# Kernel tuning notes

Hardware: AMD Instinct MI355X
Metric: run time of the kernel (lower is better)

Reference implementation:

```python
import jax, jax.numpy as jnp
import numpy as np

N = 100000   # nodes
E = 1600000  # edges
DIN = 128
HID = 128
D2 = 64      # hard-coded last-conv width in the module
OUT = 1000


def setup_inputs() -> dict:
    key = jax.random.key(0)
    ks = jax.random.split(key, 8)
    x = jax.random.normal(ks[0], (N, DIN), dtype=jnp.float32)
    edge_index = jax.random.randint(ks[1], (2, E), 0, N, dtype=jnp.int64)
    W1 = jax.random.normal(ks[2], (DIN, HID), dtype=jnp.float32) * 0.05
    b1 = jnp.zeros((HID,), dtype=jnp.float32)
    W2 = jax.random.normal(ks[3], (HID, D2), dtype=jnp.float32) * 0.05
    b2 = jnp.zeros((D2,), dtype=jnp.float32)
    Wfc = jax.random.normal(ks[4], (D2, OUT), dtype=jnp.float32) * 0.05
    bfc = jnp.zeros((OUT,), dtype=jnp.float32)
    return {"x": x, "W1": W1, "b1": b1, "W2": W2, "b2": b2,
            "Wfc": Wfc, "bfc": bfc, "edge_index": edge_index}


def _gcn_conv(x, W, b, src, dst):
    # PyG GCNConv: h = X W; add self-loops; symmetric norm D^-1/2 (A+I) D^-1/2; + bias
    h = x @ W                                   # [N, F]
    ones = jnp.ones(src.shape[0], dtype=h.dtype)
    deg = jax.ops.segment_sum(ones, dst, num_segments=N) + 1.0  # +1 for self-loop
    dinv = jax.lax.rsqrt(deg)                   # [N]
    norm = dinv[src] * dinv[dst]                # [E]
    agg = jax.ops.segment_sum(h[src] * norm[:, None], dst, num_segments=N)
    agg = agg + h * (dinv * dinv)[:, None]      # self-loop contribution
    return agg + b


def reference(x, W1, b1, W2, b2, Wfc, bfc, edge_index):
    src, dst = edge_index[0], edge_index[1]
    h = jax.nn.relu(_gcn_conv(x, W1, b1, src, dst))
    # dropout is identity in eval mode (training=False)
    h = jax.nn.relu(_gcn_conv(h, W2, b2, src, dst))
    return h @ Wfc + bfc
```

## Files before the change

### kernel.cpp

```cpp
#include <hip/hip_runtime.h>
#include <hip/hip_bf16.h>
#include <cstddef>

typedef __attribute__((ext_vector_type(8))) short bf16x8;
typedef __attribute__((ext_vector_type(4))) float f32x4;

__device__ __forceinline__ unsigned short f2bf(float f) {
    __hip_bfloat16 h = __float2bfloat16(f);
    return __builtin_bit_cast(unsigned short, h);
}
__device__ __forceinline__ float bf2f(unsigned short u) {
    return __bfloat162float(__builtin_bit_cast(__hip_bfloat16, u));
}
__device__ __forceinline__ float bflo(unsigned u) {
    return __builtin_bit_cast(float, u << 16);
}
__device__ __forceinline__ float bfhi(unsigned u) {
    return __builtin_bit_cast(float, u & 0xffff0000u);
}


__global__ void k_zero_i(int* __restrict__ p, int total) {
    int i = blockIdx.x * blockDim.x + threadIdx.x;
    int stride = gridDim.x * blockDim.x;
    for (; i < total; i += stride) p[i] = 0;
}


__global__ void k_deg_i(const int* __restrict__ dst, int* __restrict__ deg, int E) {
    int e = blockIdx.x * blockDim.x + threadIdx.x;
    if (e < E) atomicAdd(&deg[dst[e]], 1);
}

__global__ void k_dinv(const int* __restrict__ deg, float* __restrict__ dinv, int N) {
    int i = blockIdx.x * blockDim.x + threadIdx.x;
    if (i < N) dinv[i] = rsqrtf((float)deg[i] + 1.0f);
}


#define SCAN_B 1024

__global__ void k_scan1(const int* __restrict__ in, int* __restrict__ out,
                        int* __restrict__ sums, int n) {
    __shared__ int tmp[SCAN_B];
    int tid = threadIdx.x;
    int gid = blockIdx.x * SCAN_B + tid;
    int v = (gid < n) ? in[gid] : 0;
    tmp[tid] = v;
    __syncthreads();
    for (int off = 1; off < SCAN_B; off <<= 1) {
        int t = (tid >= off) ? tmp[tid - off] : 0;
        __syncthreads();
        tmp[tid] += t;
        __syncthreads();
    }
    if (gid < n) out[gid] = tmp[tid] - v;
    if (tid == SCAN_B - 1) sums[blockIdx.x] = tmp[tid];
}

__global__ void k_scan2(int* __restrict__ sums, int nb) {
    __shared__ int tmp[128];
    int tid = threadIdx.x;
    int v = (tid < nb) ? sums[tid] : 0;
    tmp[tid] = v;
    __syncthreads();
    for (int off = 1; off < 128; off <<= 1) {
        int t = (tid >= off) ? tmp[tid - off] : 0;
        __syncthreads();
        tmp[tid] += t;
        __syncthreads();
    }
    if (tid < nb) sums[tid] = tmp[tid] - v;
}

__global__ void k_scan3(int* __restrict__ out, int* __restrict__ cursor,
                        const int* __restrict__ sums, int n) {
    int gid = blockIdx.x * SCAN_B + threadIdx.x;
    if (gid < n) {
        int v = out[gid] + sums[blockIdx.x];
        out[gid] = v;
        cursor[gid] = v;
    }
}


__global__ void k_fill(const int* __restrict__ src, const int* __restrict__ dst,
                       int* __restrict__ cursor, int* __restrict__ csr_src, int E) {
    int e = blockIdx.x * blockDim.x + threadIdx.x;
    if (e < E) {
        int pos = atomicAdd(&cursor[dst[e]], 1);
        csr_src[pos] = src[e];
    }
}


__global__ void k_conv_w_bf(const float* __restrict__ W, unsigned short* __restrict__ Bh,
                            int K, int N)
{
    int n = blockIdx.x;
    int k = threadIdx.x;
    Bh[(size_t)n * K + k] = f2bf(W[(size_t)k * N + n]);
}

__global__ void k_conv_w(const float* __restrict__ W, unsigned short* __restrict__ Bh,
                         unsigned short* __restrict__ Bl, int K, int N)
{
    int n = blockIdx.x;
    int k = threadIdx.x;
    float v = W[(size_t)k * N + n];
    unsigned short hi = f2bf(v);
    unsigned short lo = f2bf(v - bf2f(hi));
    Bh[(size_t)n * K + k] = hi;
    Bl[(size_t)n * K + k] = lo;
}


__device__ __forceinline__ void unpack_fma(float* a, float w, uint4 v) {
    a[0] = fmaf(w, bflo(v.x), a[0]);
    a[1] = fmaf(w, bfhi(v.x), a[1]);
    a[2] = fmaf(w, bflo(v.y), a[2]);
    a[3] = fmaf(w, bfhi(v.y), a[3]);
    a[4] = fmaf(w, bflo(v.z), a[4]);
    a[5] = fmaf(w, bfhi(v.z), a[5]);
    a[6] = fmaf(w, bflo(v.w), a[6]);
    a[7] = fmaf(w, bfhi(v.w), a[7]);
}

__launch_bounds__(256)
__global__ void k_gather128(const unsigned short* __restrict__ hbf,
                            const int* __restrict__ csr_src, const int* __restrict__ off,
                            const float* __restrict__ dinv, const float* __restrict__ bias,
                            unsigned short* __restrict__ obf, int N, int E)
{
    int node = blockIdx.x * 4 + (threadIdx.x >> 6);
    int lane = threadIdx.x & 63;
    if (node >= N) return;
    float dn = dinv[node];
    int beg = off[node];
    int end = (node + 1 < N) ? off[node + 1] : E;

    const int grp = lane >> 4;
    const int sub = lane & 15;

    float a[8] = {0.f, 0.f, 0.f, 0.f, 0.f, 0.f, 0.f, 0.f};
    int i = beg + grp;
    for (; i + 4 < end; i += 8) {
        int s0 = csr_src[i];
        int s1 = csr_src[i + 4];
        float w0 = dinv[s0] * dn;
        float w1 = dinv[s1] * dn;
        uint4 v0 = *(const uint4*)(hbf + (size_t)s0 * 128 + sub * 8);
        uint4 v1 = *(const uint4*)(hbf + (size_t)s1 * 128 + sub * 8);
        unpack_fma(a, w0, v0);
        unpack_fma(a, w1, v1);
    }
    if (i < end) {
        int s = csr_src[i];
        float w = dinv[s] * dn;
        uint4 v = *(const uint4*)(hbf + (size_t)s * 128 + sub * 8);
        unpack_fma(a, w, v);
    }

#pragma unroll
    for (int k = 0; k < 8; ++k) {
        a[k] += __shfl_xor(a[k], 16);
        a[k] += __shfl_xor(a[k], 32);
    }

    if (grp == 0) {
        uint4 sv = *(const uint4*)(hbf + (size_t)node * 128 + sub * 8);
        float s[8] = {bflo(sv.x), bfhi(sv.x), bflo(sv.y), bfhi(sv.y),
                      bflo(sv.z), bfhi(sv.z), bflo(sv.w), bfhi(sv.w)};
        float4 b0 = *(const float4*)(bias + sub * 8);
        float4 b1 = *(const float4*)(bias + sub * 8 + 4);
        float bv[8] = {b0.x, b0.y, b0.z, b0.w, b1.x, b1.y, b1.z, b1.w};
        float w = dn * dn;
        unsigned short o[8];
#pragma unroll
        for (int k = 0; k < 8; ++k)
            o[k] = f2bf(fmaxf(fmaf(s[k], w, a[k]) + bv[k], 0.f));
        uint4 vo;
        vo.x = (unsigned)o[0] | ((unsigned)o[1] << 16);
        vo.y = (unsigned)o[2] | ((unsigned)o[3] << 16);
        vo.z = (unsigned)o[4] | ((unsigned)o[5] << 16);
        vo.w = (unsigned)o[6] | ((unsigned)o[7] << 16);
        *(uint4*)(obf + (size_t)node * 128 + sub * 8) = vo;
    }
}


__launch_bounds__(256)
__global__ void k_gather64(const unsigned short* __restrict__ hbf,
                           const int* __restrict__ csr_src, const int* __restrict__ off,
                           const float* __restrict__ dinv, const float* __restrict__ bias,
                           unsigned short* __restrict__ hhi, unsigned short* __restrict__ hlo,
                           int N, int E)
{
    int node = blockIdx.x * 4 + (threadIdx.x >> 6);
    int lane = threadIdx.x & 63;
    if (node >= N) return;
    float dn = dinv[node];
    int beg = off[node];
    int end = (node + 1 < N) ? off[node + 1] : E;

    const int grp = lane >> 3;
    const int sub = lane & 7;

    float a[8] = {0.f, 0.f, 0.f, 0.f, 0.f, 0.f, 0.f, 0.f};
    int i = beg + grp;
    for (; i + 8 < end; i += 16) {
        int s0 = csr_src[i];
        int s1 = csr_src[i + 8];
        float w0 = dinv[s0] * dn;
        float w1 = dinv[s1] * dn;
        uint4 v0 = *(const uint4*)(hbf + (size_t)s0 * 64 + sub * 8);
        uint4 v1 = *(const uint4*)(hbf + (size_t)s1 * 64 + sub * 8);
        unpack_fma(a, w0, v0);
        unpack_fma(a, w1, v1);
    }
    if (i < end) {
        int s = csr_src[i];
        float w = dinv[s] * dn;
        uint4 v = *(const uint4*)(hbf + (size_t)s * 64 + sub * 8);
        unpack_fma(a, w, v);
    }

#pragma unroll
    for (int k = 0; k < 8; ++k) {
        a[k] += __shfl_xor(a[k], 8);
        a[k] += __shfl_xor(a[k], 16);
        a[k] += __shfl_xor(a[k], 32);
    }

    if (grp == 0) {
        uint4 sv = *(const uint4*)(hbf + (size_t)node * 64 + sub * 8);
        float s[8] = {bflo(sv.x), bfhi(sv.x), bflo(sv.y), bfhi(sv.y),
                      bflo(sv.z), bfhi(sv.z), bflo(sv.w), bfhi(sv.w)};
        float4 b0 = *(const float4*)(bias + sub * 8);
        float4 b1 = *(const float4*)(bias + sub * 8 + 4);
        float bv[8] = {b0.x, b0.y, b0.z, b0.w, b1.x, b1.y, b1.z, b1.w};
        float w = dn * dn;
        unsigned short hi[8], lo[8];
#pragma unroll
        for (int k = 0; k < 8; ++k) {
            float f = fmaxf(fmaf(s[k], w, a[k]) + bv[k], 0.f);
            hi[k] = f2bf(f);
            lo[k] = f2bf(f - bf2f(hi[k]));
        }
        uint4 vh, vl;
        vh.x = (unsigned)hi[0] | ((unsigned)hi[1] << 16);
        vh.y = (unsigned)hi[2] | ((unsigned)hi[3] << 16);
        vh.z = (unsigned)hi[4] | ((unsigned)hi[5] << 16);
        vh.w = (unsigned)hi[6] | ((unsigned)hi[7] << 16);
        vl.x = (unsigned)lo[0] | ((unsigned)lo[1] << 16);
        vl.y = (unsigned)lo[2] | ((unsigned)lo[3] << 16);
        vl.z = (unsigned)lo[4] | ((unsigned)lo[5] << 16);
        vl.w = (unsigned)lo[6] | ((unsigned)lo[7] << 16);
        *(uint4*)(hhi + (size_t)node * 64 + sub * 8) = vh;
        *(uint4*)(hlo + (size_t)node * 64 + sub * 8) = vl;
    }
}


__launch_bounds__(256, 2)
__global__ void gemm_mfma_l1(const float* __restrict__ A,
                             const unsigned short* __restrict__ Bt,
                             unsigned short* __restrict__ Cbf, int M)
{
    __shared__ unsigned short Ah[128 * 64];
    __shared__ unsigned short Bh[128 * 64];

    const int tid = threadIdx.x;
    const int m0 = blockIdx.x * 128;
    const int lane = tid & 63, wave = tid >> 6;
    const int wr = wave >> 1, wc = wave & 1;
    const int lrow = lane & 15, kgrp = lane >> 4;

    f32x4 acc[4][4] = {};

    for (int ph = 0; ph < 2; ++ph) {
        const int k0 = ph * 64;
        __syncthreads();
        {
            const int c4 = tid & 15, r0 = tid >> 4;
#pragma unroll
            for (int p = 0; p < 8; ++p) {
                int row = r0 + p * 16;
                int gr = m0 + row; if (gr >= M) gr = M - 1;
                float4 v = *(const float4*)(A + (size_t)gr * 128 + k0 + c4 * 4);
                ushort4 hv;
                hv.x = f2bf(v.x); hv.y = f2bf(v.y); hv.z = f2bf(v.z); hv.w = f2bf(v.w);
                *(ushort4*)((char*)Ah + row * 128 + ((c4 * 8) ^ ((row & 7) << 4))) = hv;
            }
        }
        {
            const int c = tid & 7, col0 = tid >> 3;
#pragma unroll
            for (int p = 0; p < 4; ++p) {
                int col = col0 + p * 32;
                uint4 v = *(const uint4*)(Bt + (size_t)col * 128 + k0 + c * 8);
                *(uint4*)((char*)Bh + col * 128 + ((c * 16) ^ ((col & 7) << 4))) = v;
            }
        }
        __syncthreads();

#pragma unroll
        for (int ks = 0; ks < 2; ++ks) {
            const int cIdx = kgrp + ks * 4;
            bf16x8 ah[4], bh[4];
#pragma unroll
            for (int i = 0; i < 4; ++i) {
                int row = wr * 64 + i * 16 + lrow;
                ah[i] = *(const bf16x8*)((const char*)Ah + row * 128 + ((cIdx * 16) ^ ((row & 7) << 4)));
            }
#pragma unroll
            for (int j = 0; j < 4; ++j) {
                int col = wc * 64 + j * 16 + lrow;
                bh[j] = *(const bf16x8*)((const char*)Bh + col * 128 + ((cIdx * 16) ^ ((col & 7) << 4)));
            }
#pragma unroll
            for (int i = 0; i < 4; ++i)
#pragma unroll
                for (int j = 0; j < 4; ++j)
                    acc[i][j] = __builtin_amdgcn_mfma_f32_16x16x32_bf16(bh[j], ah[i], acc[i][j], 0, 0, 0);
        }
    }

#pragma unroll
    for (int i = 0; i < 4; ++i) {
        int grow = m0 + wr * 64 + i * 16 + lrow;
        if (grow >= M) continue;
        unsigned short* crow = Cbf + (size_t)grow * 128;
#pragma unroll
        for (int j = 0; j < 4; ++j) {
            int gc = wc * 64 + j * 16 + kgrp * 4;
            ushort4 o;
            o.x = f2bf(acc[i][j][0]);
            o.y = f2bf(acc[i][j][1]);
            o.z = f2bf(acc[i][j][2]);
            o.w = f2bf(acc[i][j][3]);
            *(ushort4*)(crow + gc) = o;
        }
    }
}


__launch_bounds__(256, 3)
__global__ void gemm_mfma_l2(const unsigned short* __restrict__ Abf,
                             const unsigned short* __restrict__ Bt,
                             unsigned short* __restrict__ Cbf, int M)
{
    __shared__ unsigned short Ah[128 * 64];
    __shared__ unsigned short Bh[64 * 64];

    const int tid = threadIdx.x;
    const int m0 = blockIdx.x * 128;
    const int lane = tid & 63, wave = tid >> 6;
    const int wr = wave >> 1, wc = wave & 1;
    const int lrow = lane & 15, kgrp = lane >> 4;

    f32x4 acc[4][2] = {};

    for (int ph = 0; ph < 2; ++ph) {
        const int k0 = ph * 64;
        __syncthreads();
        {
            const int c = tid & 7, r0 = tid >> 3;
#pragma unroll
            for (int p = 0; p < 4; ++p) {
                int row = r0 + p * 32;
                int gr = m0 + row; if (gr >= M) gr = M - 1;
                uint4 v = *(const uint4*)(Abf + (size_t)gr * 128 + k0 + c * 8);
                *(uint4*)((char*)Ah + row * 128 + ((c * 16) ^ ((row & 7) << 4))) = v;
            }
        }
        {
            const int c = tid & 7, col0 = tid >> 3;
#pragma unroll
            for (int p = 0; p < 2; ++p) {
                int col = col0 + p * 32;
                uint4 v = *(const uint4*)(Bt + (size_t)col * 128 + k0 + c * 8);
                *(uint4*)((char*)Bh + col * 128 + ((c * 16) ^ ((col & 7) << 4))) = v;
            }
        }
        __syncthreads();

#pragma unroll
        for (int ks = 0; ks < 2; ++ks) {
            const int cIdx = kgrp + ks * 4;
            bf16x8 ah[4], bh[2];
#pragma unroll
            for (int i = 0; i < 4; ++i) {
                int row = wr * 64 + i * 16 + lrow;
                ah[i] = *(const bf16x8*)((const char*)Ah + row * 128 + ((cIdx * 16) ^ ((row & 7) << 4)));
            }
#pragma unroll
            for (int j = 0; j < 2; ++j) {
                int col = wc * 32 + j * 16 + lrow;
                bh[j] = *(const bf16x8*)((const char*)Bh + col * 128 + ((cIdx * 16) ^ ((col & 7) << 4)));
            }
#pragma unroll
            for (int i = 0; i < 4; ++i)
#pragma unroll
                for (int j = 0; j < 2; ++j)
                    acc[i][j] = __builtin_amdgcn_mfma_f32_16x16x32_bf16(bh[j], ah[i], acc[i][j], 0, 0, 0);
        }
    }

#pragma unroll
    for (int i = 0; i < 4; ++i) {
        int grow = m0 + wr * 64 + i * 16 + lrow;
        if (grow >= M) continue;
        unsigned short* crow = Cbf + (size_t)grow * 64;
#pragma unroll
        for (int j = 0; j < 2; ++j) {
            int gc = wc * 32 + j * 16 + kgrp * 4;
            ushort4 o;
            o.x = f2bf(acc[i][j][0]);
            o.y = f2bf(acc[i][j][1]);
            o.z = f2bf(acc[i][j][2]);
            o.w = f2bf(acc[i][j][3]);
            *(ushort4*)(crow + gc) = o;
        }
    }
}


__launch_bounds__(256, 2)
__global__ void gemm_mfma_out(const unsigned short* __restrict__ Ahi,
                              const unsigned short* __restrict__ Alo,
                              const unsigned short* __restrict__ Bhi,
                              const unsigned short* __restrict__ Blo,
                              const float* __restrict__ bias, float* __restrict__ C,
                              int M, int N)
{
    const int tid = threadIdx.x;
    const int lane = tid & 63, wave = tid >> 6;
    const int wr = wave >> 1, wc = wave & 1;
    const int m0 = blockIdx.y * 128 + wr * 64;
    const int n0 = blockIdx.x * 128 + wc * 64;
    const int lrow = lane & 15, kgrp = lane >> 4;

    f32x4 acc[4][4] = {};

#pragma unroll
    for (int ks = 0; ks < 2; ++ks) {
        const int koff = (kgrp + ks * 4) * 8;
        bf16x8 ah[4], al[4], bh[4], bl[4];
#pragma unroll
        for (int i = 0; i < 4; ++i) {
            int row = m0 + i * 16 + lrow; if (row >= M) row = M - 1;
            ah[i] = *(const bf16x8*)(Ahi + (size_t)row * 64 + koff);
            al[i] = *(const bf16x8*)(Alo + (size_t)row * 64 + koff);
        }
#pragma unroll
        for (int j = 0; j < 4; ++j) {
            int col = n0 + j * 16 + lrow; if (col >= N) col = N - 1;
            bh[j] = *(const bf16x8*)(Bhi + (size_t)col * 64 + koff);
            bl[j] = *(const bf16x8*)(Blo + (size_t)col * 64 + koff);
        }
#pragma unroll
        for (int i = 0; i < 4; ++i)
#pragma unroll
            for (int j = 0; j < 4; ++j) {
                acc[i][j] = __builtin_amdgcn_mfma_f32_16x16x32_bf16(bh[j], ah[i], acc[i][j], 0, 0, 0);
                acc[i][j] = __builtin_amdgcn_mfma_f32_16x16x32_bf16(bl[j], ah[i], acc[i][j], 0, 0, 0);
                acc[i][j] = __builtin_amdgcn_mfma_f32_16x16x32_bf16(bh[j], al[i], acc[i][j], 0, 0, 0);
            }
    }

#pragma unroll
    for (int i = 0; i < 4; ++i) {
        int grow = m0 + i * 16 + lrow;
        if (grow >= M) continue;
        float* crow = C + (size_t)grow * N;
#pragma unroll
        for (int j = 0; j < 4; ++j) {
            int gc = n0 + j * 16 + kgrp * 4;
            if (gc + 4 <= N) {
                float4 bv = *(const float4*)(bias + gc);
                *(float4*)(crow + gc) = make_float4(acc[i][j][0] + bv.x,
                                                    acc[i][j][1] + bv.y,
                                                    acc[i][j][2] + bv.z,
                                                    acc[i][j][3] + bv.w);
            }
        }
    }
}


extern "C" void kernel_launch(void* const* d_in, const int* in_sizes, int n_in,
                              void* d_out, int out_size, void* d_ws, size_t ws_size,
                              hipStream_t stream)
{
    const float* x   = (const float*)d_in[0];
    const float* W1  = (const float*)d_in[1];
    const float* b1  = (const float*)d_in[2];
    const float* W2  = (const float*)d_in[3];
    const float* b2  = (const float*)d_in[4];
    const float* Wfc = (const float*)d_in[5];
    const float* bfc = (const float*)d_in[6];
    const int*   ei  = (const int*)d_in[7];

    const int Nn = in_sizes[0] / 128;
    const int E  = in_sizes[7] / 2;
    const int* src = ei;
    const int* dst = ei + E;

    char* ws = (char*)d_ws;
    float*          dinv   = (float*)(ws);
    unsigned short* Wfc_hi = (unsigned short*)(ws + 512 * 1024);
    unsigned short* Wfc_lo = (unsigned short*)(ws + 768 * 1024);
    unsigned short* W1_bf  = (unsigned short*)(ws + 1024 * 1024);
    unsigned short* W2_bf  = (unsigned short*)(ws + 1088 * 1024);
    unsigned short* h2hi   = (unsigned short*)(ws + 1152 * 1024);
    unsigned short* h2lo   = (unsigned short*)(ws + 1152 * 1024 + (size_t)Nn * 64 * 2);

    char* ob = (char*)d_out;
    unsigned short* hbf     = (unsigned short*)ob;
    unsigned short* h1bf    = (unsigned short*)(ob + (size_t)Nn * 256);
    unsigned short* h2bf    = (unsigned short*)(ob + (size_t)Nn * 512);
    int*            csr_src = (int*)(ob + (size_t)Nn * 640);
    int*            offs    = (int*)((char*)csr_src + (size_t)E * 4);
    int*            cursor  = (int*)((char*)offs + (size_t)Nn * 4);
    int*            deg_cnt = (int*)((char*)cursor + (size_t)Nn * 4);
    int*            bsums   = (int*)((char*)deg_cnt + (size_t)Nn * 4);

    const int nScanBlocks = (Nn + SCAN_B - 1) / SCAN_B;

    k_zero_i<<<128, 256, 0, stream>>>(deg_cnt, Nn);
    k_deg_i<<<(E + 255) / 256, 256, 0, stream>>>(dst, deg_cnt, E);
    k_dinv<<<(Nn + 255) / 256, 256, 0, stream>>>(deg_cnt, dinv, Nn);
    k_scan1<<<nScanBlocks, SCAN_B, 0, stream>>>(deg_cnt, offs, bsums, Nn);
    k_scan2<<<1, 128, 0, stream>>>(bsums, nScanBlocks);
    k_scan3<<<nScanBlocks, SCAN_B, 0, stream>>>(offs, cursor, bsums, Nn);
    k_fill<<<(E + 255) / 256, 256, 0, stream>>>(src, dst, cursor, csr_src, E);
    k_conv_w_bf<<<128, 128, 0, stream>>>(W1, W1_bf, 128, 128);
    k_conv_w_bf<<<64, 128, 0, stream>>>(W2, W2_bf, 128, 64);
    k_conv_w<<<1000, 64, 0, stream>>>(Wfc, Wfc_hi, Wfc_lo, 64, 1000);

    gemm_mfma_l1<<<dim3((Nn + 127) / 128, 1), 256, 0, stream>>>(x, W1_bf, hbf, Nn);
    k_gather128<<<(Nn + 3) / 4, 256, 0, stream>>>(hbf, csr_src, offs, dinv, b1,
                                                  h1bf, Nn, E);

    gemm_mfma_l2<<<dim3((Nn + 127) / 128, 1), 256, 0, stream>>>(h1bf, W2_bf, h2bf, Nn);
    k_gather64<<<(Nn + 3) / 4, 256, 0, stream>>>(h2bf, csr_src, offs, dinv, b2,
                                                 h2hi, h2lo, Nn, E);

    gemm_mfma_out<<<dim3((1000 + 127) / 128, (Nn + 127) / 128), 256, 0, stream>>>(
        h2hi, h2lo, Wfc_hi, Wfc_lo, bfc, (float*)d_out, Nn, 1000);
}
```

Measured before the change: 529.1 us.

## Fuse dinv into scan, unroll gather loop, hoist self loads, raise out-GEMM occupancy

Result: no change. 523.9 us (-1.0%).

```diff
diff --git a/kernel.cpp b/kernel.cpp
--- a/kernel.cpp
+++ b/kernel.cpp
@@ -32,20 +32,16 @@
     if (e < E) atomicAdd(&deg[dst[e]], 1);
 }
 
-__global__ void k_dinv(const int* __restrict__ deg, float* __restrict__ dinv, int N) {
-    int i = blockIdx.x * blockDim.x + threadIdx.x;
-    if (i < N) dinv[i] = rsqrtf((float)deg[i] + 1.0f);
-}
-
 
 #define SCAN_B 1024
 
 __global__ void k_scan1(const int* __restrict__ in, int* __restrict__ out,
-                        int* __restrict__ sums, int n) {
+                        int* __restrict__ sums, float* __restrict__ dinv, int n) {
     __shared__ int tmp[SCAN_B];
     int tid = threadIdx.x;
     int gid = blockIdx.x * SCAN_B + tid;
     int v = (gid < n) ? in[gid] : 0;
+    if (gid < n) dinv[gid] = rsqrtf((float)v + 1.0f);
     tmp[tid] = v;
     __syncthreads();
     for (int off = 1; off < SCAN_B; off <<= 1) {
@@ -142,19 +138,35 @@
     const int grp = lane >> 4;
     const int sub = lane & 15;
 
+    uint4 sv = make_uint4(0, 0, 0, 0);
+    float4 b0 = make_float4(0.f, 0.f, 0.f, 0.f), b1 = b0;
+    if (grp == 0) {
+        sv = *(const uint4*)(hbf + (size_t)node * 128 + sub * 8);
+        b0 = *(const float4*)(bias + sub * 8);
+        b1 = *(const float4*)(bias + sub * 8 + 4);
+    }
+
     float a[8] = {0.f, 0.f, 0.f, 0.f, 0.f, 0.f, 0.f, 0.f};
     int i = beg + grp;
-    for (; i + 4 < end; i += 8) {
+    for (; i + 12 < end; i += 16) {
         int s0 = csr_src[i];
         int s1 = csr_src[i + 4];
+        int s2 = csr_src[i + 8];
+        int s3 = csr_src[i + 12];
         float w0 = dinv[s0] * dn;
         float w1 = dinv[s1] * dn;
+        float w2 = dinv[s2] * dn;
+        float w3 = dinv[s3] * dn;
         uint4 v0 = *(const uint4*)(hbf + (size_t)s0 * 128 + sub * 8);
         uint4 v1 = *(const uint4*)(hbf + (size_t)s1 * 128 + sub * 8);
+        uint4 v2 = *(const uint4*)(hbf + (size_t)s2 * 128 + sub * 8);
+        uint4 v3 = *(const uint4*)(hbf + (size_t)s3 * 128 + sub * 8);
         unpack_fma(a, w0, v0);
         unpack_fma(a, w1, v1);
-    }
-    if (i < end) {
+        unpack_fma(a, w2, v2);
+        unpack_fma(a, w3, v3);
+    }
+    for (; i < end; i += 4) {
         int s = csr_src[i];
         float w = dinv[s] * dn;
         uint4 v = *(const uint4*)(hbf + (size_t)s * 128 + sub * 8);
@@ -168,11 +180,8 @@
     }
 
     if (grp == 0) {
-        uint4 sv = *(const uint4*)(hbf + (size_t)node * 128 + sub * 8);
         float s[8] = {bflo(sv.x), bfhi(sv.x), bflo(sv.y), bfhi(sv.y),
                       bflo(sv.z), bfhi(sv.z), bflo(sv.w), bfhi(sv.w)};
-        float4 b0 = *(const float4*)(bias + sub * 8);
-        float4 b1 = *(const float4*)(bias + sub * 8 + 4);
         float bv[8] = {b0.x, b0.y, b0.z, b0.w, b1.x, b1.y, b1.z, b1.w};
         float w = dn * dn;
         unsigned short o[8];
@@ -205,6 +214,14 @@
 
     const int grp = lane >> 3;
     const int sub = lane & 7;
+
+    uint4 sv = make_uint4(0, 0, 0, 0);
+    float4 b0 = make_float4(0.f, 0.f, 0.f, 0.f), b1 = b0;
+    if (grp == 0) {
+        sv = *(const uint4*)(hbf + (size_t)node * 64 + sub * 8);
+        b0 = *(const float4*)(bias + sub * 8);
+        b1 = *(const float4*)(bias + sub * 8 + 4);
+    }
 
     float a[8] = {0.f, 0.f, 0.f, 0.f, 0.f, 0.f, 0.f, 0.f};
     int i = beg + grp;
@@ -233,11 +250,8 @@
     }
 
     if (grp == 0) {
-        uint4 sv = *(const uint4*)(hbf + (size_t)node * 64 + sub * 8);
         float s[8] = {bflo(sv.x), bfhi(sv.x), bflo(sv.y), bfhi(sv.y),
                       bflo(sv.z), bfhi(sv.z), bflo(sv.w), bfhi(sv.w)};
-        float4 b0 = *(const float4*)(bias + sub * 8);
-        float4 b1 = *(const float4*)(bias + sub * 8 + 4);
         float bv[8] = {b0.x, b0.y, b0.z, b0.w, b1.x, b1.y, b1.z, b1.w};
         float w = dn * dn;
         unsigned short hi[8], lo[8];
@@ -426,7 +440,7 @@
 }
 
 
-__launch_bounds__(256, 2)
+__launch_bounds__(256, 3)
 __global__ void gemm_mfma_out(const unsigned short* __restrict__ Ahi,
                               const unsigned short* __restrict__ Alo,
                               const unsigned short* __restrict__ Bhi,
@@ -530,8 +544,7 @@
 
     k_zero_i<<<128, 256, 0, stream>>>(deg_cnt, Nn);
     k_deg_i<<<(E + 255) / 256, 256, 0, stream>>>(dst, deg_cnt, E);
-    k_dinv<<<(Nn + 255) / 256, 256, 0, stream>>>(deg_cnt, dinv, Nn);
-    k_scan1<<<nScanBlocks, SCAN_B, 0, stream>>>(deg_cnt, offs, bsums, Nn);
+    k_scan1<<<nScanBlocks, SCAN_B, 0, stream>>>(deg_cnt, offs, bsums, dinv, Nn);
     k_scan2<<<1, 128, 0, stream>>>(bsums, nScanBlocks);
     k_scan3<<<nScanBlocks, SCAN_B, 0, stream>>>(offs, cursor, bsums, Nn);
     k_fill<<<(E + 255) / 256, 256, 0, stream>>>(src, dst, cursor, csr_src, E);
```
